# Performance work log

Measured on AMD Instinct MI355X. Metric: run time of the kernel, lower is better.

The kernel has to match this reference:

```python
import jax, jax.numpy as jnp
import numpy as np

D_MODEL, H, D_FF = 512, 8, 2048
B, S = 2, 2048
EPS = 1e-6


def _layernorm(x, alpha, beta):
    # Faithful to the torch module: unbiased std (ddof=1), eps added to STD,
    # scalar alpha/beta parameters.
    m = jnp.mean(x, axis=-1, keepdims=True)
    var = jnp.sum((x - m) ** 2, axis=-1, keepdims=True) / (x.shape[-1] - 1)
    std = jnp.sqrt(var)
    return alpha * (x - m) / (std + EPS) + beta


def _mha(x, mask, Wq, bq, Wk, bk, Wv, bv, Wo, bo):
    Bn, Sn, D = x.shape
    dk = D // H
    q = (x @ Wq + bq).reshape(Bn, Sn, H, dk).transpose(0, 2, 1, 3)  # [B,H,S,dk]
    k = (x @ Wk + bk).reshape(Bn, Sn, H, dk).transpose(0, 2, 1, 3)
    v = (x @ Wv + bv).reshape(Bn, Sn, H, dk).transpose(0, 2, 1, 3)
    scores = jnp.einsum('bhqd,bhkd->bhqk', q, k) / jnp.sqrt(jnp.float32(dk))
    scores = jnp.where(mask == 0, -jnp.inf, scores)  # mask [B,1,1,S] broadcasts
    attn = jax.nn.softmax(scores, axis=-1)
    out = jnp.einsum('bhqk,bhkd->bhqd', attn, v)
    out = out.transpose(0, 2, 1, 3).reshape(Bn, Sn, D)
    return out @ Wo + bo


def _ffn(x, W1, b1, W2, b2):
    return jax.nn.relu(x @ W1 + b1) @ W2 + b2


def setup_inputs() -> dict:
    key = jax.random.key(0)
    ks = jax.random.split(key, 12)
    sd = 1.0 / np.sqrt(D_MODEL)
    sdf = 1.0 / np.sqrt(D_FF)
    inp = {
        'x': jax.random.normal(ks[0], (B, S, D_MODEL), jnp.float32),
        'src_mask': jnp.ones((B, 1, 1, S), jnp.int32),
        'Wq': jax.random.normal(ks[1], (D_MODEL, D_MODEL), jnp.float32) * sd,
        'bq': jnp.zeros((D_MODEL,), jnp.float32),
        'Wk': jax.random.normal(ks[2], (D_MODEL, D_MODEL), jnp.float32) * sd,
        'bk': jnp.zeros((D_MODEL,), jnp.float32),
        'Wv': jax.random.normal(ks[3], (D_MODEL, D_MODEL), jnp.float32) * sd,
        'bv': jnp.zeros((D_MODEL,), jnp.float32),
        'Wo': jax.random.normal(ks[4], (D_MODEL, D_MODEL), jnp.float32) * sd,
        'bo': jnp.zeros((D_MODEL,), jnp.float32),
        'W1': jax.random.normal(ks[5], (D_MODEL, D_FF), jnp.float32) * sd,
        'b1': jnp.zeros((D_FF,), jnp.float32),
        'W2': jax.random.normal(ks[6], (D_FF, D_MODEL), jnp.float32) * sdf,
        'b2': jnp.zeros((D_MODEL,), jnp.float32),
        'alpha1': jnp.ones((1,), jnp.float32),
        'beta1': jnp.zeros((1,), jnp.float32),
        'alpha2': jnp.ones((1,), jnp.float32),
        'beta2': jnp.zeros((1,), jnp.float32),
    }
    return inp


def reference(x, src_mask, Wq, bq, Wk, bk, Wv, bv, Wo, bo,
              W1, b1, W2, b2, alpha1, beta1, alpha2, beta2):
    # SkipConnection 0: x + dropout(MHA(LN(x)))  (dropout=0 -> identity)
    h1 = _layernorm(x, alpha1, beta1)
    x = x + _mha(h1, src_mask, Wq, bq, Wk, bk, Wv, bv, Wo, bo)
    # SkipConnection 1: x + dropout(FFN(LN(x)))
    h2 = _layernorm(x, alpha2, beta2)
    x = x + _ffn(h2, W1, b1, W2, b2)
    return x
```

## Files before the change

### kernel.cpp

```cpp
#include <hip/hip_runtime.h>
#include <hip/hip_bf16.h>

typedef __hip_bfloat16 bf16;
typedef __attribute__((ext_vector_type(8))) short s8v;
typedef __attribute__((ext_vector_type(4))) float f32x4;

#define DM 512
#define NH 8
#define DKH 64
#define DFF 2048
#define NB 2
#define NS 2048
#define NR (NB*NS)
#define LN_EPS 1e-6f
#define NEG_BIG (-1e30f)
#define LDQKV (3*DM)
#define SM_SCALE2 0.18033688f
#define SM_SHIFT2 (-8.656170245f)
#define PART_ELEMS (NB*NH*NS*DKH)

#define MFMA_B16(a,b,c) __builtin_amdgcn_mfma_f32_16x16x32_bf16(a,b,c,0,0,0)

#define GLOAD16(g, l) __builtin_amdgcn_global_load_lds( \
    (const __attribute__((address_space(1))) void*)(g), \
    (__attribute__((address_space(3))) void*)(l), 16, 0, 0)

__device__ __forceinline__ float us2f(unsigned int u){ return __uint_as_float(u << 16); }
__device__ __forceinline__ float b2f(bf16 v){ return __bfloat162float(v); }
__device__ __forceinline__ float ldf(const float* p){ return *p; }
__device__ __forceinline__ float ldf(const bf16* p){ return __bfloat162float(*p); }
__device__ __forceinline__ void stf(float* p, float v){ *p = v; }
__device__ __forceinline__ void stf(bf16* p, float v){ *p = __float2bfloat16(v); }

__device__ __forceinline__ int swz(int row, int colbyte){
  return ((row<<7) + colbyte) ^ ((row&7)<<4);
}

__device__ __forceinline__ float wsum(float v){
#pragma unroll
  for(int o=32;o>0;o>>=1) v += __shfl_down(v,o,64);
  return v;
}

__device__ __forceinline__ void stage_tile(char* lds, const bf16* g, int ld, int R, int tid){
  int wave = tid>>6, lane = tid&63;
  int nch = R*8;
  for(int c0 = wave*64; c0 < nch; c0 += 256){
    int c = c0 + lane;
    int row = c>>3;
    int blk = (c&7) ^ (row&7);
    GLOAD16(g + (size_t)row*ld + blk*8, lds + c0*16);
  }
}
__device__ __forceinline__ s8v read_frag(const char* lds, int row, int col){
  return *reinterpret_cast<const s8v*>(lds + swz(row, col<<1));
}

template<typename TI>
__global__ __launch_bounds__(256) void ln_kernel(const TI* __restrict__ x,
    bf16* __restrict__ out, const float* __restrict__ ap, const float* __restrict__ bp){
  __shared__ float s1[4], s2[4];
  int row = blockIdx.x, tid = threadIdx.x;
  const TI* xr = x + (size_t)row*DM;
  float v0 = ldf(xr+tid), v1 = ldf(xr+tid+256);
  float s = wsum(v0+v1);
  float q = wsum(v0*v0+v1*v1);
  int wid = tid>>6, lane = tid&63;
  if(lane==0){ s1[wid]=s; s2[wid]=q; }
  __syncthreads();
  float S = s1[0]+s1[1]+s1[2]+s1[3];
  float Q = s2[0]+s2[1]+s2[2]+s2[3];
  float mean = S*(1.f/DM);
  float var  = (Q - (float)DM*mean*mean)*(1.f/(DM-1));
  float sd   = sqrtf(fmaxf(var,0.f));
  float sc = (*ap)/(sd+LN_EPS);
  float b = *bp;
  bf16* orow = out + (size_t)row*DM;
  orow[tid]     = __float2bfloat16((v0-mean)*sc + b);
  orow[tid+256] = __float2bfloat16((v1-mean)*sc + b);
}

__global__ __launch_bounds__(256) void transpose_all(
    const float* __restrict__ Wq, const float* __restrict__ Wk,
    const float* __restrict__ Wv, const float* __restrict__ Wo,
    const float* __restrict__ W1, const float* __restrict__ W2,
    bf16* __restrict__ WTqkv, bf16* __restrict__ WTo,
    bf16* __restrict__ WT1, bf16* __restrict__ WT2){
  __shared__ float t[64][65];
  int tb = blockIdx.x;
  const float* W; bf16* WT; int K, N, nx;
  if(tb < 192){
    int w = tb>>6; tb &= 63;
    W = (w==0)?Wq:(w==1)?Wk:Wv; WT = WTqkv + w*512*512; K=512; N=512; nx=8;
  } else if(tb < 256){ tb -= 192; W=Wo; WT=WTo; K=512; N=512; nx=8; }
  else if(tb < 512){ tb -= 256; W=W1; WT=WT1; K=512; N=2048; nx=32; }
  else { tb -= 512; W=W2; WT=WT2; K=2048; N=512; nx=8; }
  int n0 = (tb % nx)*64, k0 = (tb / nx)*64;
  int tid = threadIdx.x;
  int rr = tid>>6, cc = tid&63;
#pragma unroll
  for(int r=rr;r<64;r+=4) t[r][cc] = W[(size_t)(k0+r)*N + n0+cc];
  __syncthreads();
#pragma unroll
  for(int r=rr;r<64;r+=4) WT[(size_t)(n0+r)*K + k0+cc] = __float2bfloat16(t[cc][r]);
}

__global__ __launch_bounds__(256) void transpose_v(const bf16* __restrict__ Vg,
    bf16* __restrict__ VT){
  __shared__ float t[64][65];
  int tid = threadIdx.x;
  int s0 = blockIdx.x*64; int bh = blockIdx.y;
  int b = bh>>3, h = bh&7;
  int rr = tid>>6, cc = tid&63;
#pragma unroll
  for(int r=rr;r<64;r+=4)
    t[r][cc] = b2f(Vg[((size_t)(b*NS + s0+r))*LDQKV + h*DKH + cc]);
  __syncthreads();
#pragma unroll
  for(int r=rr;r<64;r+=4)
    VT[((size_t)bh*DKH + r)*NS + s0+cc] = __float2bfloat16(t[cc][r]);
}

template<int BM, int BN, int DBUF, int RELU, int QKVSEL, typename TR, typename TO>
__global__ __launch_bounds__(256) void mfma_gemm(
    const bf16* __restrict__ A, const bf16* __restrict__ WT,
    const float* __restrict__ bias0, const float* __restrict__ bias1,
    const float* __restrict__ bias2,
    const TR* __restrict__ resid, TO* __restrict__ out, int M, int N, int K){
  constexpr int NW = BN/2, NF = NW/16, MI = BM/32, WRS = BM/2;
  __shared__ char lA[1+DBUF][BM*128];
  __shared__ char lB[1+DBUF][BN*128];
  int tid = threadIdx.x, wave = tid>>6, lane = tid&63;
  int m0 = blockIdx.x*BM, n0 = blockIdx.y*BN;
  int wr = wave>>1, wc = wave&1;
  int g = lane>>4, li = lane&15;
  f32x4 acc[MI][NF] = {};
  if(DBUF){
    stage_tile(lA[0], A + (size_t)m0*K, K, BM, tid);
    stage_tile(lB[0], WT + (size_t)n0*K, K, BN, tid);
    __syncthreads();
  }
  int cur = 0;
  for(int kt=0; kt<K; kt+=64, cur^=DBUF){
    if(!DBUF){
      stage_tile(lA[0], A + (size_t)m0*K + kt, K, BM, tid);
      stage_tile(lB[0], WT + (size_t)n0*K + kt, K, BN, tid);
      __syncthreads();
    } else if(kt+64 < K){
      stage_tile(lA[cur^1], A + (size_t)m0*K + kt+64, K, BM, tid);
      stage_tile(lB[cur^1], WT + (size_t)n0*K + kt+64, K, BN, tid);
    }
#pragma unroll
    for(int kk=0; kk<2; kk++){
      s8v af[MI], bfr[NF];
#pragma unroll
      for(int mi=0;mi<MI;mi++) af[mi] = read_frag(lA[cur], wr*WRS+mi*16+li, kk*32+g*8);
#pragma unroll
      for(int ni=0;ni<NF;ni++) bfr[ni] = read_frag(lB[cur], wc*NW+ni*16+li, kk*32+g*8);
#pragma unroll
      for(int mi=0;mi<MI;mi++)
#pragma unroll
        for(int ni=0;ni<NF;ni++)
          acc[mi][ni] = MFMA_B16(af[mi], bfr[ni], acc[mi][ni]);
    }
    __syncthreads();
  }
#pragma unroll
  for(int mi=0;mi<MI;mi++)
#pragma unroll
  for(int ni=0;ni<NF;ni++){
    int row = m0 + wr*WRS + mi*16 + g*4;
    int col = n0 + wc*NW + ni*16 + li;
    const float* bp = bias0;
    if(QKVSEL) bp = (col<512)? bias0 : (col<1024)? (bias1-512) : (bias2-1024);
    float bb = bp[col];
#pragma unroll
    for(int r=0;r<4;r++){
      float v = acc[mi][ni][r] + bb;
      if(RELU) v = fmaxf(v, 0.f);
      size_t off = (size_t)(row+r)*N + col;
      if(resid) v += ldf(resid+off);
      stf(out+off, v);
    }
  }
}

__global__ __launch_bounds__(256,4) void flash_attn(
    const bf16* __restrict__ QKV, const bf16* __restrict__ VT,
    const int* __restrict__ mask, bf16* __restrict__ partA,
    bf16* __restrict__ partB, float* __restrict__ lbuf){
  __shared__ char lK[2][64*128];
  __shared__ char lV[2][64*128];
  __shared__ char lP[4][16*128];
  int tid = threadIdx.x, wave = tid>>6, lane = tid&63;
  int q0 = blockIdx.x*64, h = blockIdx.y;
  int b = blockIdx.z>>1, kh = blockIdx.z&1;
  int kbase = kh*(NS/2);
  int g = lane>>4, li = lane&15;
  const bf16* Qg  = QKV + ((size_t)b*NS + q0)*LDQKV + h*DKH;
  const bf16* Kg  = QKV + ((size_t)b*NS + kbase)*LDQKV + DM + h*DKH;
  const bf16* VTg = VT + ((size_t)(b*NH + h))*DKH*NS + kbase;
  stage_tile(lK[0], Qg, LDQKV, 64, tid);
  __syncthreads();
  s8v qf0 = read_frag(lK[0], wave*16+li, g*8);
  s8v qf1 = read_frag(lK[0], wave*16+li, 32+g*8);
  __syncthreads();
  stage_tile(lK[0], Kg, LDQKV, 64, tid);
  stage_tile(lV[0], VTg, NS, 64, tid);
  unsigned long long mb = 0;
#pragma unroll 16
  for(int j=0;j<64;j++)
    mb |= (unsigned long long)(mask[b*NS + kbase + j*16 + li] != 0) << j;
  __syncthreads();
  f32x4 acc[4] = {};
  f32x4 acc_l = {};
  s8v ones;
#pragma unroll
  for(int j=0;j<8;j++) ones[j] = (short)0x3F80;
  char* lPw = lP[wave];

  auto compute = [&](int kt, int c){
    f32x4 S[4] = {};
#pragma unroll
    for(int kk=0;kk<2;kk++){
      s8v qf = kk ? qf1 : qf0;
      s8v kf[4];
#pragma unroll
      for(int ni=0;ni<4;ni++) kf[ni] = read_frag(lK[c], ni*16+li, kk*32+g*8);
#pragma unroll
      for(int ni=0;ni<4;ni++)
        S[ni] = MFMA_B16(qf, kf[ni], S[ni]);
    }
    int jb = kt>>4;
    float madd[4];
#pragma unroll
    for(int ni=0;ni<4;ni++)
      madd[ni] = ((mb>>(jb+ni))&1ull) ? SM_SHIFT2 : NEG_BIG;
#pragma unroll
    for(int r=0;r<4;r++){
      float e0 = exp2f(fmaf(S[0][r], SM_SCALE2, madd[0]));
      float e1 = exp2f(fmaf(S[1][r], SM_SCALE2, madd[1]));
      float e2 = exp2f(fmaf(S[2][r], SM_SCALE2, madd[2]));
      float e3 = exp2f(fmaf(S[3][r], SM_SCALE2, madd[3]));
      int row = g*4 + r;
      *reinterpret_cast<bf16*>(lPw + swz(row, (0*16+li)<<1)) = __float2bfloat16(e0);
      *reinterpret_cast<bf16*>(lPw + swz(row, (1*16+li)<<1)) = __float2bfloat16(e1);
      *reinterpret_cast<bf16*>(lPw + swz(row, (2*16+li)<<1)) = __float2bfloat16(e2);
      *reinterpret_cast<bf16*>(lPw + swz(row, (3*16+li)<<1)) = __float2bfloat16(e3);
    }
#pragma unroll
    for(int kk=0;kk<2;kk++){
      s8v pf = read_frag(lPw, li, kk*32+g*8);
      s8v vf[4];
#pragma unroll
      for(int nd=0;nd<4;nd++) vf[nd] = read_frag(lV[c], nd*16+li, kk*32+g*8);
#pragma unroll
      for(int nd=0;nd<4;nd++)
        acc[nd] = MFMA_B16(pf, vf[nd], acc[nd]);
      acc_l = MFMA_B16(pf, ones, acc_l);
    }
  };

  int cur = 0;
  for(int t=0; t<15; ++t, cur^=1){
    stage_tile(lK[cur^1], Kg + (size_t)(t+1)*64*LDQKV, LDQKV, 64, tid);
    stage_tile(lV[cur^1], VTg + (t+1)*64, NS, 64, tid);
    asm volatile("s_waitcnt vmcnt(4)" ::: "memory");
    __builtin_amdgcn_sched_barrier(0);
    __builtin_amdgcn_s_barrier();
    compute(t*64, cur);
    __builtin_amdgcn_s_barrier();
  }
  asm volatile("s_waitcnt vmcnt(0)" ::: "memory");
  __builtin_amdgcn_sched_barrier(0);
  __builtin_amdgcn_s_barrier();
  compute(15*64, cur);

  bf16* part = kh ? partB : partA;
  size_t qb = (size_t)(b*NH + h)*NS;
#pragma unroll
  for(int r=0;r<4;r++){
    int qrow = q0 + wave*16 + g*4 + r;
#pragma unroll
    for(int nd=0;nd<4;nd++)
      part[(qb + qrow)*DKH + nd*16 + li] = __float2bfloat16(acc[nd][r]);
    if(li==0)
      lbuf[((size_t)((b*NH+h)*2 + kh))*NS + qrow] = acc_l[r];
  }
}

__global__ __launch_bounds__(256) void combine_attn(const bf16* __restrict__ pA,
    const bf16* __restrict__ pB, const float* __restrict__ lbuf,
    bf16* __restrict__ cx){
  int e = blockIdx.x*256 + threadIdx.x;
  int idx = e*4;
  int d = idx & 63, q = (idx>>6)&(NS-1), h = (idx>>17)&7, b = idx>>20;
  uint2 ua = *reinterpret_cast<const uint2*>(pA+idx);
  uint2 ub = *reinterpret_cast<const uint2*>(pB+idx);
  float lA = lbuf[((size_t)((b*NH+h)*2+0))*NS + q];
  float lB = lbuf[((size_t)((b*NH+h)*2+1))*NS + q];
  float il = 1.f/(lA+lB);
  bf16* o = cx + ((size_t)(b*NS+q)*DM + h*DKH + d);
  o[0] = __float2bfloat16((us2f(ua.x&0xffffu)+us2f(ub.x&0xffffu))*il);
  o[1] = __float2bfloat16((us2f(ua.x>>16)+us2f(ub.x>>16))*il);
  o[2] = __float2bfloat16((us2f(ua.y&0xffffu)+us2f(ub.y&0xffffu))*il);
  o[3] = __float2bfloat16((us2f(ua.y>>16)+us2f(ub.y>>16))*il);
}

extern "C" void kernel_launch(void* const* d_in, const int* in_sizes, int n_in,
                              void* d_out, int out_size, void* d_ws, size_t ws_size,
                              hipStream_t stream){
  const float* x   = (const float*)d_in[0];
  const int* mask  = (const int*)d_in[1];
  const float* Wq = (const float*)d_in[2];
  const float* bq = (const float*)d_in[3];
  const float* Wk = (const float*)d_in[4];
  const float* bk = (const float*)d_in[5];
  const float* Wv = (const float*)d_in[6];
  const float* bv = (const float*)d_in[7];
  const float* Wo = (const float*)d_in[8];
  const float* bo = (const float*)d_in[9];
  const float* W1 = (const float*)d_in[10];
  const float* b1 = (const float*)d_in[11];
  const float* W2 = (const float*)d_in[12];
  const float* b2 = (const float*)d_in[13];
  const float* a1 = (const float*)d_in[14];
  const float* be1= (const float*)d_in[15];
  const float* a2 = (const float*)d_in[16];
  const float* be2= (const float*)d_in[17];

  char* ws = (char*)d_ws;
  bf16* h1    = (bf16*)(ws);
  bf16* accA  = (bf16*)(ws);
  bf16* WTqkv = (bf16*)(ws + (size_t)( 4<<20));
  bf16* WTo   = (bf16*)(ws + (size_t)(11<<19));
  bf16* WT1   = (bf16*)(ws + (size_t)( 8<<20));
  bf16* WT2   = (bf16*)(ws + (size_t)(10<<20));
  bf16* qkv   = (bf16*)(ws + (size_t)(12<<20));
  bf16* VT    = (bf16*)(ws + (size_t)(24<<20));
  bf16* cx    = (bf16*)(ws + (size_t)(24<<20));
  bf16* x1    = h1;
  bf16* h2    = (bf16*)(ws + (size_t)( 4<<20));
  bf16* mid   = qkv;
  float* lbuf = (float*)d_out;
  bf16* accB  = (bf16*)((char*)d_out + (1<<20));

  transpose_all<<<768,256,0,stream>>>(Wq,Wk,Wv,Wo,W1,W2, WTqkv,WTo,WT1,WT2);

  ln_kernel<float><<<NR,256,0,stream>>>(x, h1, a1, be1);
  mfma_gemm<128,64,1,0,1,float,bf16><<<dim3(32,24),256,0,stream>>>(
      h1, WTqkv, bq, bk, bv, (const float*)nullptr, qkv, NR, LDQKV, DM);
  transpose_v<<<dim3(32,16),256,0,stream>>>(qkv + 2*DM, VT);
  flash_attn<<<dim3(NS/64,NH,NB*2),256,0,stream>>>(qkv, VT, mask, accA, accB, lbuf);
  combine_attn<<<PART_ELEMS/1024,256,0,stream>>>(accA, accB, lbuf, cx);
  mfma_gemm<64,64,1,0,0,float,bf16><<<dim3(64,8),256,0,stream>>>(
      cx, WTo, bo, bo, bo, x, x1, NR, DM, DM);
  ln_kernel<bf16><<<NR,256,0,stream>>>(x1, h2, a2, be2);
  mfma_gemm<128,128,0,1,0,float,bf16><<<dim3(32,16),256,0,stream>>>(
      h2, WT1, b1, b1, b1, (const float*)nullptr, mid, NR, DFF, DM);
  mfma_gemm<64,64,1,0,0,bf16,float><<<dim3(64,8),256,0,stream>>>(
      mid, WT2, b2, b2, b2, x1, (float*)d_out, NR, DM, DFF);
}
```

Baseline: 142.7 us.

## Pipeline GEMM tile loads with vmcnt waits and vectorize P stores

The GEMM kernel now always double-buffers its LDS tiles and issues the next tile's async global-to-LDS loads before computing. It waits with a targeted vmcnt count and raw s_barrier instead of a full __syncthreads, so loads overlap MFMA work; the FFN1 GEMM previously ran single-buffered. In attention, the V transpose permutes key positions so each lane can write its four exp values as one 8-byte LDS store instead of four 2-byte stores. The vmcnt constants assume a fixed number of loads per thread per stage, and the key permutation must stay consistent between the P and V layouts.

```diff
diff --git a/kernel.cpp b/kernel.cpp
--- a/kernel.cpp
+++ b/kernel.cpp
@@ -31,6 +31,17 @@
 __device__ __forceinline__ float ldf(const bf16* p){ return __bfloat162float(*p); }
 __device__ __forceinline__ void stf(float* p, float v){ *p = v; }
 __device__ __forceinline__ void stf(bf16* p, float v){ *p = __float2bfloat16(v); }
+__device__ __forceinline__ unsigned short f2bu(float f){
+  bf16 b = __float2bfloat16(f);
+  return *reinterpret_cast<unsigned short*>(&b);
+}
+
+template<int N> __device__ __forceinline__ void waitcnt_vm(){
+  if constexpr(N==0)      asm volatile("s_waitcnt vmcnt(0)" ::: "memory");
+  else if constexpr(N==4) asm volatile("s_waitcnt vmcnt(4)" ::: "memory");
+  else if constexpr(N==6) asm volatile("s_waitcnt vmcnt(6)" ::: "memory");
+  else if constexpr(N==8) asm volatile("s_waitcnt vmcnt(8)" ::: "memory");
+}
 
 __device__ __forceinline__ int swz(int row, int colbyte){
   return ((row<<7) + colbyte) ^ ((row&7)<<4);
@@ -116,40 +127,42 @@
   for(int r=rr;r<64;r+=4)
     t[r][cc] = b2f(Vg[((size_t)(b*NS + s0+r))*LDQKV + h*DKH + cc]);
   __syncthreads();
+  int kp = (cc&15)*4 + (cc>>4);
 #pragma unroll
   for(int r=rr;r<64;r+=4)
-    VT[((size_t)bh*DKH + r)*NS + s0+cc] = __float2bfloat16(t[cc][r]);
-}
-
-template<int BM, int BN, int DBUF, int RELU, int QKVSEL, typename TR, typename TO>
+    VT[((size_t)bh*DKH + r)*NS + s0 + kp] = __float2bfloat16(t[cc][r]);
+}
+
+template<int BM, int BN, int RELU, int QKVSEL, typename TR, typename TO>
 __global__ __launch_bounds__(256) void mfma_gemm(
     const bf16* __restrict__ A, const bf16* __restrict__ WT,
     const float* __restrict__ bias0, const float* __restrict__ bias1,
     const float* __restrict__ bias2,
     const TR* __restrict__ resid, TO* __restrict__ out, int M, int N, int K){
   constexpr int NW = BN/2, NF = NW/16, MI = BM/32, WRS = BM/2;
-  __shared__ char lA[1+DBUF][BM*128];
-  __shared__ char lB[1+DBUF][BN*128];
+  constexpr int LOADS = BM/32 + BN/32;
+  __shared__ char lA[2][BM*128];
+  __shared__ char lB[2][BN*128];
   int tid = threadIdx.x, wave = tid>>6, lane = tid&63;
   int m0 = blockIdx.x*BM, n0 = blockIdx.y*BN;
   int wr = wave>>1, wc = wave&1;
   int g = lane>>4, li = lane&15;
   f32x4 acc[MI][NF] = {};
-  if(DBUF){
-    stage_tile(lA[0], A + (size_t)m0*K, K, BM, tid);
-    stage_tile(lB[0], WT + (size_t)n0*K, K, BN, tid);
-    __syncthreads();
-  }
+  stage_tile(lA[0], A + (size_t)m0*K, K, BM, tid);
+  stage_tile(lB[0], WT + (size_t)n0*K, K, BN, tid);
+  int NT = K>>6;
   int cur = 0;
-  for(int kt=0; kt<K; kt+=64, cur^=DBUF){
-    if(!DBUF){
-      stage_tile(lA[0], A + (size_t)m0*K + kt, K, BM, tid);
-      stage_tile(lB[0], WT + (size_t)n0*K + kt, K, BN, tid);
-      __syncthreads();
-    } else if(kt+64 < K){
-      stage_tile(lA[cur^1], A + (size_t)m0*K + kt+64, K, BM, tid);
-      stage_tile(lB[cur^1], WT + (size_t)n0*K + kt+64, K, BN, tid);
-    }
+  for(int t=0; t<NT; ++t, cur^=1){
+    if(t+1 < NT){
+      stage_tile(lA[cur^1], A + (size_t)m0*K + (t+1)*64, K, BM, tid);
+      stage_tile(lB[cur^1], WT + (size_t)n0*K + (t+1)*64, K, BN, tid);
+      waitcnt_vm<LOADS>();
+    } else {
+      waitcnt_vm<0>();
+    }
+    __builtin_amdgcn_sched_barrier(0);
+    __builtin_amdgcn_s_barrier();
+    __builtin_amdgcn_sched_barrier(0);
 #pragma unroll
     for(int kk=0; kk<2; kk++){
       s8v af[MI], bfr[NF];
@@ -163,7 +176,8 @@
         for(int ni=0;ni<NF;ni++)
           acc[mi][ni] = MFMA_B16(af[mi], bfr[ni], acc[mi][ni]);
     }
-    __syncthreads();
+    __builtin_amdgcn_sched_barrier(0);
+    __builtin_amdgcn_s_barrier();
   }
 #pragma unroll
   for(int mi=0;mi<MI;mi++)
@@ -243,10 +257,10 @@
       float e2 = exp2f(fmaf(S[2][r], SM_SCALE2, madd[2]));
       float e3 = exp2f(fmaf(S[3][r], SM_SCALE2, madd[3]));
       int row = g*4 + r;
-      *reinterpret_cast<bf16*>(lPw + swz(row, (0*16+li)<<1)) = __float2bfloat16(e0);
-      *reinterpret_cast<bf16*>(lPw + swz(row, (1*16+li)<<1)) = __float2bfloat16(e1);
-      *reinterpret_cast<bf16*>(lPw + swz(row, (2*16+li)<<1)) = __float2bfloat16(e2);
-      *reinterpret_cast<bf16*>(lPw + swz(row, (3*16+li)<<1)) = __float2bfloat16(e3);
+      uint2 w;
+      w.x = (unsigned int)f2bu(e0) | ((unsigned int)f2bu(e1)<<16);
+      w.y = (unsigned int)f2bu(e2) | ((unsigned int)f2bu(e3)<<16);
+      *reinterpret_cast<uint2*>(lPw + swz(row, li<<3)) = w;
     }
 #pragma unroll
     for(int kk=0;kk<2;kk++){
@@ -265,15 +279,18 @@
   for(int t=0; t<15; ++t, cur^=1){
     stage_tile(lK[cur^1], Kg + (size_t)(t+1)*64*LDQKV, LDQKV, 64, tid);
     stage_tile(lV[cur^1], VTg + (t+1)*64, NS, 64, tid);
-    asm volatile("s_waitcnt vmcnt(4)" ::: "memory");
+    waitcnt_vm<4>();
     __builtin_amdgcn_sched_barrier(0);
     __builtin_amdgcn_s_barrier();
+    __builtin_amdgcn_sched_barrier(0);
     compute(t*64, cur);
+    __builtin_amdgcn_sched_barrier(0);
     __builtin_amdgcn_s_barrier();
   }
-  asm volatile("s_waitcnt vmcnt(0)" ::: "memory");
+  waitcnt_vm<0>();
   __builtin_amdgcn_sched_barrier(0);
   __builtin_amdgcn_s_barrier();
+  __builtin_amdgcn_sched_barrier(0);
   compute(15*64, cur);
 
   bf16* part = kh ? partB : partA;
@@ -348,16 +365,16 @@
   transpose_all<<<768,256,0,stream>>>(Wq,Wk,Wv,Wo,W1,W2, WTqkv,WTo,WT1,WT2);
 
   ln_kernel<float><<<NR,256,0,stream>>>(x, h1, a1, be1);
-  mfma_gemm<128,64,1,0,1,float,bf16><<<dim3(32,24),256,0,stream>>>(
+  mfma_gemm<128,64,0,1,float,bf16><<<dim3(32,24),256,0,stream>>>(
       h1, WTqkv, bq, bk, bv, (const float*)nullptr, qkv, NR, LDQKV, DM);
   transpose_v<<<dim3(32,16),256,0,stream>>>(qkv + 2*DM, VT);
   flash_attn<<<dim3(NS/64,NH,NB*2),256,0,stream>>>(qkv, VT, mask, accA, accB, lbuf);
   combine_attn<<<PART_ELEMS/1024,256,0,stream>>>(accA, accB, lbuf, cx);
-  mfma_gemm<64,64,1,0,0,float,bf16><<<dim3(64,8),256,0,stream>>>(
+  mfma_gemm<64,64,0,0,float,bf16><<<dim3(64,8),256,0,stream>>>(
       cx, WTo, bo, bo, bo, x, x1, NR, DM, DM);
   ln_kernel<bf16><<<NR,256,0,stream>>>(x1, h2, a2, be2);
-  mfma_gemm<128,128,0,1,0,float,bf16><<<dim3(32,16),256,0,stream>>>(
+  mfma_gemm<128,128,1,0,float,bf16><<<dim3(32,16),256,0,stream>>>(
       h2, WT1, b1, b1, b1, (const float*)nullptr, mid, NR, DFF, DM);
-  mfma_gemm<64,64,1,0,0,bf16,float><<<dim3(64,8),256,0,stream>>>(
+  mfma_gemm<64,64,0,0,bf16,float><<<dim3(64,8),256,0,stream>>>(
       mid, WT2, b2, b2, b2, x1, (float*)d_out, NR, DM, DFF);
 }
```

After: 142.0 us. No clear change (-0.5%).
